# Performance work log

Measured on AMD Instinct MI355X. Metric: run time of the kernel, lower is better.

## Reference

```python
import jax, jax.numpy as jnp
import numpy as np

N, E, F, D = 50000, 800000, 128, 32
CUTOFF = 5.0


def swish(x):
    return x * jax.nn.sigmoid(x)


def setup_inputs() -> dict:
    key = jax.random.key(0)
    ks = jax.random.split(key, 15)
    sF = 1.0 / np.sqrt(F)
    inp = {
        "x": jax.random.normal(ks[0], (N, F), jnp.float32),
        # distances in [0, 6) so some edges lie beyond the 5.0 cutoff
        "rij": jax.random.uniform(ks[1], (E,), jnp.float32) * 6.0,
        "vij": jax.random.normal(ks[2], (E, 3), jnp.float32),
        "src": jax.random.randint(ks[3], (E,), 0, N),
        "dst": jax.random.randint(ks[4], (E,), 0, N),
        # transform: Dense(F,F,swish) -> Dense(F,D,swish)
        "W1": jax.random.normal(ks[5], (F, F), jnp.float32) * sF,
        "b1": jnp.zeros((F,), jnp.float32),
        "W2": jax.random.normal(ks[6], (F, D), jnp.float32) * sF,
        "b2": jnp.zeros((D,), jnp.float32),
        # transform2 (cross_product branch)
        "W1b": jax.random.normal(ks[7], (F, F), jnp.float32) * sF,
        "b1b": jnp.zeros((F,), jnp.float32),
        "W2b": jax.random.normal(ks[8], (F, D), jnp.float32) * sF,
        "b2b": jnp.zeros((D,), jnp.float32),
        # mix: Dense(3, 1), no activation
        "w_mix": jax.random.normal(ks[9], (3,), jnp.float32) * (1.0 / np.sqrt(3.0)),
        "b_mix": jnp.zeros((1,), jnp.float32),
    }
    return inp


def reference(x, rij, vij, src, dst, W1, b1, W2, b2, W1b, b1b, W2b, b2b, w_mix, b_mix):
    # node transforms: q, q2 in [N, D]
    q = swish(swish(x @ W1 + b1) @ W2 + b2)
    q2 = swish(swish(x @ W1b + b1b) @ W2b + b2b)

    # cosine cutoff on per-edge distance [E]
    c = 0.5 * (jnp.cos(jnp.pi * rij / CUTOFF) + 1.0)
    c = c * (rij < CUTOFF).astype(c.dtype)

    # e_mul_u: edge vij [E,1,3] * source-node q [E,D,1] -> [E,D,3], then cutoff scale
    mu_ij = vij[:, None, :] * q[src][:, :, None] * c[:, None, None]
    mu = jax.ops.segment_sum(mu_ij, dst, num_segments=N)  # [N,D,3]

    mu_ij2 = vij[:, None, :] * q2[src][:, :, None] * c[:, None, None]
    mu2 = jax.ops.segment_sum(mu_ij2, dst, num_segments=N)  # [N,D,3]

    mu3 = jnp.cross(mu, mu2, axis=-1)  # [N,D,3]
    stacked = jnp.stack([mu, mu2, mu3], axis=-1)  # [N,D,3,3]
    out = stacked @ w_mix + b_mix[0]  # mix Dense(3,1), squeezed -> [N,D,3]
    return out
```

## Files before the change

kernel.cpp:

```cpp
#include <hip/hip_runtime.h>
#include <hip/hip_bf16.h>

#define N_NODES 50000
#define E_EDGES 800000
#define F_DIM 128
#define D_DIM 32
#define CUTOFF 5.0f
#define PI_F 3.14159265358979f
#define SCAN_BLOCKS ((N_NODES + 255) / 256)

#define MLP_BLOCKS ((N_NODES + 31) / 32)
#define HIST_BLOCKS ((E_EDGES + 255) / 256)
#define XPAD 132
#define SQ_STRIDE 66

__device__ __forceinline__ float swishf(float x) { return x / (1.0f + expf(-x)); }

__global__ __launch_bounds__(256, 4)
void mlp_hist(const float* __restrict__ x,
              const float* __restrict__ W1a, const float* __restrict__ b1a,
              const float* __restrict__ W2a, const float* __restrict__ b2a,
              const float* __restrict__ W1b, const float* __restrict__ b1b,
              const float* __restrict__ W2b, const float* __restrict__ b2b,
              float* __restrict__ qq,
              const float* __restrict__ rij, const int* __restrict__ dst,
              int* __restrict__ deg) {
  if (blockIdx.x >= MLP_BLOCKS) {
    const int e = (blockIdx.x - MLP_BLOCKS) * 256 + threadIdx.x;
    if (e < E_EDGES && rij[e] < CUTOFF) atomicAdd(&deg[dst[e]], 1);
    return;
  }

  __shared__ float sX[64 * XPAD];

  const int rb = blockIdx.x * 32;
  const int t  = threadIdx.x;
  const int w  = t >> 6;
  const int l  = t & 63;

  {
    const int row = t >> 3;
    const int kq  = t & 7;
    const int rowG = min(rb + row, N_NODES - 1);
    const float* xp = x + (size_t)rowG * F_DIM;
#pragma unroll
    for (int p = 0; p < 4; ++p) {
      const int k0 = kq * 4 + p * 32;
      *(float4*)&sX[row * XPAD + k0] = *(const float4*)&xp[k0];
    }
  }
  __syncthreads();

  const int h1    = l >> 5;
  const int cl    = l & 31;
  const int col   = w * 32 + cl;
  const int rbase = h1 * 16;

  float accA[16], accB[16];
  {
    const float bA = b1a[col];
    const float bB = b1b[col];
#pragma unroll
    for (int r = 0; r < 16; ++r) { accA[r] = bA; accB[r] = bB; }
  }
  {
    const float* xrow = sX + rbase * XPAD;
#pragma unroll 2
    for (int k4 = 0; k4 < 32; ++k4) {
      float wa[4], wb[4];
#pragma unroll
      for (int kk = 0; kk < 4; ++kk) {
        const size_t off = (size_t)(k4 * 4 + kk) * F_DIM + col;
        wa[kk] = W1a[off];
        wb[kk] = W1b[off];
      }
#pragma unroll
      for (int r = 0; r < 16; ++r) {
        const float4 xv = *(const float4*)&xrow[r * XPAD + k4 * 4];
        accA[r] = fmaf(xv.x, wa[0], accA[r]);
        accA[r] = fmaf(xv.y, wa[1], accA[r]);
        accA[r] = fmaf(xv.z, wa[2], accA[r]);
        accA[r] = fmaf(xv.w, wa[3], accA[r]);
        accB[r] = fmaf(xv.x, wb[0], accB[r]);
        accB[r] = fmaf(xv.y, wb[1], accB[r]);
        accB[r] = fmaf(xv.z, wb[2], accB[r]);
        accB[r] = fmaf(xv.w, wb[3], accB[r]);
      }
    }
  }

  __syncthreads();
#pragma unroll
  for (int r = 0; r < 16; ++r) {
    sX[(rbase + r) * XPAD + col]      = swishf(accA[r]);
    sX[(32 + rbase + r) * XPAD + col] = swishf(accB[r]);
  }
  __syncthreads();

  const int s   = w * 16 + (l & 15);
  const int rq  = l >> 4;
  const int br2 = s >> 5;
  const int c2  = s & 31;

  const float* __restrict__ W2 = br2 ? W2b : W2a;
  const float* hbase = sX + (br2 ? 32 : 0) * XPAD + (rq * 8) * XPAD;

  float acc2[8];
  {
    const float b2v = (br2 ? b2b : b2a)[c2];
#pragma unroll
    for (int r = 0; r < 8; ++r) acc2[r] = b2v;
  }
#pragma unroll 2
  for (int k4 = 0; k4 < 32; ++k4) {
    float w2v[4];
#pragma unroll
    for (int kk = 0; kk < 4; ++kk)
      w2v[kk] = W2[(size_t)(k4 * 4 + kk) * D_DIM + c2];
#pragma unroll
    for (int r = 0; r < 8; ++r) {
      const float4 hv = *(const float4*)&hbase[r * XPAD + k4 * 4];
      acc2[r] = fmaf(hv.x, w2v[0], acc2[r]);
      acc2[r] = fmaf(hv.y, w2v[1], acc2[r]);
      acc2[r] = fmaf(hv.z, w2v[2], acc2[r]);
      acc2[r] = fmaf(hv.w, w2v[3], acc2[r]);
    }
  }

  __syncthreads();
#pragma unroll
  for (int r = 0; r < 8; ++r)
    sX[(rq * 8 + r) * SQ_STRIDE + 2 * c2 + br2] = swishf(acc2[r]);
  __syncthreads();

  {
    const int row = t >> 3;
    const int m   = t & 7;
    if (rb + row < N_NODES) {
      const float* sq = &sX[row * SQ_STRIDE + m * 8];
      float4 v0 = *(const float4*)&sq[0];
      float4 v1 = *(const float4*)&sq[4];
      float* qp = &qq[(size_t)(rb + row) * 64 + m * 8];
      *(float4*)&qp[0] = v0;
      *(float4*)&qp[4] = v1;
    }
  }
}

__global__ __launch_bounds__(256)
void scan_blocksum(const int* __restrict__ deg, int* __restrict__ part) {
  __shared__ int red[256];
  const int t = threadIdx.x;
  const int i = blockIdx.x * 256 + t;
  red[t] = (i < N_NODES) ? deg[i] : 0;
  __syncthreads();
#pragma unroll
  for (int off = 128; off > 0; off >>= 1) {
    if (t < off) red[t] += red[t + off];
    __syncthreads();
  }
  if (t == 0) part[blockIdx.x] = red[0];
}

__global__ __launch_bounds__(256)
void scan_finish(const int* __restrict__ deg, const int* __restrict__ part,
                 int* __restrict__ row_start, int* __restrict__ cursor) {
  __shared__ int sp[256];
  __shared__ int s[256];
  const int t = threadIdx.x;
  sp[t] = (t < SCAN_BLOCKS) ? part[t] : 0;
  __syncthreads();
  for (int off = 1; off < 256; off <<= 1) {
    const int u = (t >= off) ? sp[t - off] : 0;
    __syncthreads();
    sp[t] += u;
    __syncthreads();
  }
  const int bofs = (blockIdx.x > 0) ? sp[blockIdx.x - 1] : 0;
  if (blockIdx.x == 0 && t == 0) row_start[N_NODES] = sp[SCAN_BLOCKS - 1];

  const int i = blockIdx.x * 256 + t;
  const int v = (i < N_NODES) ? deg[i] : 0;
  s[t] = v;
  __syncthreads();
  for (int off = 1; off < 256; off <<= 1) {
    const int u = (t >= off) ? s[t - off] : 0;
    __syncthreads();
    s[t] += u;
    __syncthreads();
  }
  const int excl = s[t] - v + bofs;
  if (i < N_NODES) { row_start[i] = excl; cursor[i] = excl; }
}

__global__ __launch_bounds__(256)
void edge_reorder(const float* __restrict__ rij, const float* __restrict__ vij,
                  const int* __restrict__ src, const int* __restrict__ dst,
                  int* __restrict__ cursor, float4* __restrict__ recs) {
  const int e = blockIdx.x * 256 + threadIdx.x;
  if (e >= E_EDGES) return;
  const float r = rij[e];
  if (r >= CUTOFF) return;
  const float c = 0.5f * (cosf(r * (PI_F / CUTOFF)) + 1.0f);
  const int pos = atomicAdd(&cursor[dst[e]], 1);
  recs[pos] = make_float4(c * vij[3 * e + 0], c * vij[3 * e + 1],
                          c * vij[3 * e + 2], __int_as_float(src[e]));
}

__global__ __launch_bounds__(256)
void gather_out(const int* __restrict__ row_start, const float4* __restrict__ recs,
                const float2* __restrict__ qq,
                const float* __restrict__ w_mix, const float* __restrict__ b_mix,
                float* __restrict__ out) {
  const int tid = blockIdx.x * 256 + threadIdx.x;
  const int n = tid >> 5;
  const int d = tid & 31;
  if (n >= N_NODES) return;

  const int s0 = row_start[n];
  const int s1 = row_start[n + 1];

  float ax = 0.f, ay = 0.f, az = 0.f, bx = 0.f, by = 0.f, bz = 0.f;
  for (int i = s0; i < s1; i += 4) {
    const int i1 = min(i + 1, s1 - 1);
    const int i2 = min(i + 2, s1 - 1);
    const int i3 = min(i + 3, s1 - 1);
    float4 rc0 = recs[i];
    float4 rc1 = recs[i1];
    float4 rc2 = recs[i2];
    float4 rc3 = recs[i3];
    float2 p0 = qq[__float_as_int(rc0.w) * 32 + d];
    float2 p1 = qq[__float_as_int(rc1.w) * 32 + d];
    float2 p2 = qq[__float_as_int(rc2.w) * 32 + d];
    float2 p3 = qq[__float_as_int(rc3.w) * 32 + d];
    const float m1 = (i + 1 < s1) ? 1.f : 0.f;
    const float m2 = (i + 2 < s1) ? 1.f : 0.f;
    const float m3 = (i + 3 < s1) ? 1.f : 0.f;
    p1.x *= m1; p1.y *= m1;
    p2.x *= m2; p2.y *= m2;
    p3.x *= m3; p3.y *= m3;

    ax += rc0.x * p0.x + rc1.x * p1.x + rc2.x * p2.x + rc3.x * p3.x;
    ay += rc0.y * p0.x + rc1.y * p1.x + rc2.y * p2.x + rc3.y * p3.x;
    az += rc0.z * p0.x + rc1.z * p1.x + rc2.z * p2.x + rc3.z * p3.x;
    bx += rc0.x * p0.y + rc1.x * p1.y + rc2.x * p2.y + rc3.x * p3.y;
    by += rc0.y * p0.y + rc1.y * p1.y + rc2.y * p2.y + rc3.y * p3.y;
    bz += rc0.z * p0.y + rc1.z * p1.y + rc2.z * p2.y + rc3.z * p3.y;
  }

  const float cx = ay * bz - az * by;
  const float cy = az * bx - ax * bz;
  const float cz = ax * by - ay * bx;

  const float w0 = w_mix[0], w1 = w_mix[1], w2 = w_mix[2];
  const float bm = b_mix[0];

  const size_t base = (size_t)tid * 3;
  out[base + 0] = ax * w0 + bx * w1 + cx * w2 + bm;
  out[base + 1] = ay * w0 + by * w1 + cy * w2 + bm;
  out[base + 2] = az * w0 + bz * w1 + cz * w2 + bm;
}

extern "C" void kernel_launch(void* const* d_in, const int* in_sizes, int n_in,
                              void* d_out, int out_size, void* d_ws, size_t ws_size,
                              hipStream_t stream) {
  const float* x     = (const float*)d_in[0];
  const float* rij   = (const float*)d_in[1];
  const float* vij   = (const float*)d_in[2];
  const int*   src   = (const int*)  d_in[3];
  const int*   dst   = (const int*)  d_in[4];
  const float* W1    = (const float*)d_in[5];
  const float* b1    = (const float*)d_in[6];
  const float* W2    = (const float*)d_in[7];
  const float* b2    = (const float*)d_in[8];
  const float* W1b   = (const float*)d_in[9];
  const float* b1b   = (const float*)d_in[10];
  const float* W2b   = (const float*)d_in[11];
  const float* b2b   = (const float*)d_in[12];
  const float* w_mix = (const float*)d_in[13];
  const float* b_mix = (const float*)d_in[14];
  float* out = (float*)d_out;

  float4* recs   = (float4*)d_ws;
  float* qq      = (float*)(recs + E_EDGES);
  int* deg       = (int*)(qq + (size_t)N_NODES * 64);
  int* cursor    = deg + N_NODES;
  int* row_start = cursor + N_NODES;
  int* part      = row_start + N_NODES + 1;

  hipMemsetAsync(deg, 0, sizeof(int) * N_NODES, stream);

  mlp_hist<<<MLP_BLOCKS + HIST_BLOCKS, 256, 0, stream>>>(
      x, W1, b1, W2, b2, W1b, b1b, W2b, b2b, qq, rij, dst, deg);

  scan_blocksum<<<SCAN_BLOCKS, 256, 0, stream>>>(deg, part);
  scan_finish<<<SCAN_BLOCKS, 256, 0, stream>>>(deg, part, row_start, cursor);

  const int eb = (E_EDGES + 255) / 256;
  edge_reorder<<<eb, 256, 0, stream>>>(rij, vij, src, dst, cursor, recs);

  gather_out<<<(N_NODES * D_DIM) / 256, 256, 0, stream>>>(
      row_start, recs, (const float2*)qq, w_mix, b_mix, out);
}
```

Measured before the change: 285.4 us.

## Run node MLP on bf16 MFMA with split hi/lo precision emulation

Replaces the scalar FP32 FMA loops of both MLP layers with MFMA 16x16x32 bf16 matrix instructions. Accuracy is kept close to fp32 by splitting each operand into bf16 hi and lo parts and using three MFMAs per tile. A new prep kernel converts and transposes the weights into hi/lo bf16 buffers and also zeroes the degree array, replacing the memset. The weight buffers live in the workspace region aliased with the tail of the edge-record buffer, which is safe only because edge_reorder writes recs after the MLP has run.

New measurement: 240.2 us. 15.8% less time.

```diff
diff --git a/kernel.cpp b/kernel.cpp
--- a/kernel.cpp
+++ b/kernel.cpp
@@ -11,17 +11,53 @@
 
 #define MLP_BLOCKS ((N_NODES + 31) / 32)
 #define HIST_BLOCKS ((E_EDGES + 255) / 256)
-#define XPAD 132
-#define SQ_STRIDE 66
+#define XS 136
+#define HS 264
+
+typedef __attribute__((ext_vector_type(8))) short bf16x8;
+typedef __attribute__((ext_vector_type(4))) float f32x4;
 
 __device__ __forceinline__ float swishf(float x) { return x / (1.0f + expf(-x)); }
+
+__device__ __forceinline__ unsigned short f2bf(float v) {
+  unsigned u = __float_as_uint(v);
+  u += 0x7FFFu + ((u >> 16) & 1u);
+  return (unsigned short)(u >> 16);
+}
+__device__ __forceinline__ float bf2f(unsigned short h) {
+  return __uint_as_float(((unsigned)h) << 16);
+}
+
+__global__ __launch_bounds__(256)
+void prep(const float* __restrict__ W1a, const float* __restrict__ W1b,
+          const float* __restrict__ W2a, const float* __restrict__ W2b,
+          unsigned short* __restrict__ w1hi, unsigned short* __restrict__ w1lo,
+          unsigned short* __restrict__ w2hi, unsigned short* __restrict__ w2lo,
+          int* __restrict__ deg) {
+  const int id = blockIdx.x * 256 + threadIdx.x;
+  if (id < N_NODES) deg[id] = 0;
+  if (id < 2 * 128 * 128) {
+    const int b = id >> 14, rem = id & 16383, c = rem >> 7, k = rem & 127;
+    const float v = (b ? W1b : W1a)[k * F_DIM + c];
+    const unsigned short h = f2bf(v);
+    w1hi[id] = h;
+    w1lo[id] = f2bf(v - bf2f(h));
+  }
+  if (id < 2 * 32 * 128) {
+    const int b = id >> 12, rem = id & 4095, c = rem >> 7, k = rem & 127;
+    const float v = (b ? W2b : W2a)[k * D_DIM + c];
+    const unsigned short h = f2bf(v);
+    w2hi[id] = h;
+    w2lo[id] = f2bf(v - bf2f(h));
+  }
+}
 
 __global__ __launch_bounds__(256, 4)
 void mlp_hist(const float* __restrict__ x,
-              const float* __restrict__ W1a, const float* __restrict__ b1a,
-              const float* __restrict__ W2a, const float* __restrict__ b2a,
-              const float* __restrict__ W1b, const float* __restrict__ b1b,
-              const float* __restrict__ W2b, const float* __restrict__ b2b,
+              const unsigned short* __restrict__ w1hi, const unsigned short* __restrict__ w1lo,
+              const unsigned short* __restrict__ w2hi, const unsigned short* __restrict__ w2lo,
+              const float* __restrict__ b1a, const float* __restrict__ b1b,
+              const float* __restrict__ b2a, const float* __restrict__ b2b,
               float* __restrict__ qq,
               const float* __restrict__ rij, const int* __restrict__ dst,
               int* __restrict__ deg) {
@@ -31,12 +67,17 @@
     return;
   }
 
-  __shared__ float sX[64 * XPAD];
+  __shared__ unsigned short sU[2 * 32 * HS];
 
   const int rb = blockIdx.x * 32;
   const int t  = threadIdx.x;
   const int w  = t >> 6;
   const int l  = t & 63;
+  const int lr = l & 15;
+  const int kb = l >> 4;
+
+  unsigned short* xh = sU;
+  unsigned short* xl = sU + 32 * XS;
 
   {
     const int row = t >> 3;
@@ -46,100 +87,120 @@
 #pragma unroll
     for (int p = 0; p < 4; ++p) {
       const int k0 = kq * 4 + p * 32;
-      *(float4*)&sX[row * XPAD + k0] = *(const float4*)&xp[k0];
-    }
-  }
-  __syncthreads();
-
-  const int h1    = l >> 5;
-  const int cl    = l & 31;
-  const int col   = w * 32 + cl;
-  const int rbase = h1 * 16;
-
-  float accA[16], accB[16];
+      const float4 v = *(const float4*)&xp[k0];
+      ushort4 hi4, lo4;
+      hi4.x = f2bf(v.x); lo4.x = f2bf(v.x - bf2f(hi4.x));
+      hi4.y = f2bf(v.y); lo4.y = f2bf(v.y - bf2f(hi4.y));
+      hi4.z = f2bf(v.z); lo4.z = f2bf(v.z - bf2f(hi4.z));
+      hi4.w = f2bf(v.w); lo4.w = f2bf(v.w - bf2f(hi4.w));
+      *(ushort4*)&xh[row * XS + k0] = hi4;
+      *(ushort4*)&xl[row * XS + k0] = lo4;
+    }
+  }
+  __syncthreads();
+
+  f32x4 acc[2][4];
+#pragma unroll
+  for (int mt = 0; mt < 2; ++mt)
+#pragma unroll
+    for (int ct = 0; ct < 4; ++ct) acc[mt][ct] = (f32x4){0.f, 0.f, 0.f, 0.f};
+
+#pragma unroll
+  for (int ks = 0; ks < 4; ++ks) {
+    bf16x8 ah[2], al[2];
+#pragma unroll
+    for (int mt = 0; mt < 2; ++mt) {
+      ah[mt] = *(const bf16x8*)&xh[(mt * 16 + lr) * XS + ks * 32 + kb * 8];
+      al[mt] = *(const bf16x8*)&xl[(mt * 16 + lr) * XS + ks * 32 + kb * 8];
+    }
+#pragma unroll
+    for (int ct = 0; ct < 4; ++ct) {
+      const int cb = w * 64 + ct * 16;
+      const size_t wo = (size_t)(cb + lr) * 128 + ks * 32 + kb * 8;
+      const bf16x8 bh = *(const bf16x8*)&w1hi[wo];
+      const bf16x8 bl = *(const bf16x8*)&w1lo[wo];
+#pragma unroll
+      for (int mt = 0; mt < 2; ++mt) {
+        acc[mt][ct] = __builtin_amdgcn_mfma_f32_16x16x32_bf16(ah[mt], bh, acc[mt][ct], 0, 0, 0);
+        acc[mt][ct] = __builtin_amdgcn_mfma_f32_16x16x32_bf16(ah[mt], bl, acc[mt][ct], 0, 0, 0);
+        acc[mt][ct] = __builtin_amdgcn_mfma_f32_16x16x32_bf16(al[mt], bh, acc[mt][ct], 0, 0, 0);
+      }
+    }
+  }
+
+  __syncthreads();
+  unsigned short* hh = sU;
+  unsigned short* hl = sU + 32 * HS;
+
   {
-    const float bA = b1a[col];
-    const float bB = b1b[col];
-#pragma unroll
-    for (int r = 0; r < 16; ++r) { accA[r] = bA; accB[r] = bB; }
-  }
-  {
-    const float* xrow = sX + rbase * XPAD;
-#pragma unroll 2
-    for (int k4 = 0; k4 < 32; ++k4) {
-      float wa[4], wb[4];
-#pragma unroll
-      for (int kk = 0; kk < 4; ++kk) {
-        const size_t off = (size_t)(k4 * 4 + kk) * F_DIM + col;
-        wa[kk] = W1a[off];
-        wb[kk] = W1b[off];
+    const float* b1p = (w >= 2) ? b1b : b1a;
+#pragma unroll
+    for (int ct = 0; ct < 4; ++ct) {
+      const int colc = w * 64 + ct * 16 + lr;
+      const float bias = b1p[colc & 127];
+#pragma unroll
+      for (int mt = 0; mt < 2; ++mt) {
+#pragma unroll
+        for (int rg = 0; rg < 4; ++rg) {
+          const int rowr = mt * 16 + kb * 4 + rg;
+          const float hv = swishf(acc[mt][ct][rg] + bias);
+          const unsigned short hb = f2bf(hv);
+          hh[rowr * HS + colc] = hb;
+          hl[rowr * HS + colc] = f2bf(hv - bf2f(hb));
+        }
       }
-#pragma unroll
-      for (int r = 0; r < 16; ++r) {
-        const float4 xv = *(const float4*)&xrow[r * XPAD + k4 * 4];
-        accA[r] = fmaf(xv.x, wa[0], accA[r]);
-        accA[r] = fmaf(xv.y, wa[1], accA[r]);
-        accA[r] = fmaf(xv.z, wa[2], accA[r]);
-        accA[r] = fmaf(xv.w, wa[3], accA[r]);
-        accB[r] = fmaf(xv.x, wb[0], accB[r]);
-        accB[r] = fmaf(xv.y, wb[1], accB[r]);
-        accB[r] = fmaf(xv.z, wb[2], accB[r]);
-        accB[r] = fmaf(xv.w, wb[3], accB[r]);
-      }
-    }
-  }
-
-  __syncthreads();
-#pragma unroll
-  for (int r = 0; r < 16; ++r) {
-    sX[(rbase + r) * XPAD + col]      = swishf(accA[r]);
-    sX[(32 + rbase + r) * XPAD + col] = swishf(accB[r]);
-  }
-  __syncthreads();
-
-  const int s   = w * 16 + (l & 15);
-  const int rq  = l >> 4;
-  const int br2 = s >> 5;
-  const int c2  = s & 31;
-
-  const float* __restrict__ W2 = br2 ? W2b : W2a;
-  const float* hbase = sX + (br2 ? 32 : 0) * XPAD + (rq * 8) * XPAD;
-
-  float acc2[8];
+    }
+  }
+  __syncthreads();
+
+  const int cb2 = 16 * w;
+  const int br2 = cb2 >> 5;
+  const int c2  = (cb2 & 31) + lr;
+
+  f32x4 acc2[2];
+  acc2[0] = (f32x4){0.f, 0.f, 0.f, 0.f};
+  acc2[1] = (f32x4){0.f, 0.f, 0.f, 0.f};
+#pragma unroll
+  for (int ks = 0; ks < 4; ++ks) {
+    bf16x8 ah2[2], al2[2];
+#pragma unroll
+    for (int mt = 0; mt < 2; ++mt) {
+      const int ho = (mt * 16 + lr) * HS + br2 * 128 + ks * 32 + kb * 8;
+      ah2[mt] = *(const bf16x8*)&hh[ho];
+      al2[mt] = *(const bf16x8*)&hl[ho];
+    }
+    const size_t w2o = (size_t)(br2 * 32 + c2) * 128 + ks * 32 + kb * 8;
+    const bf16x8 bh2 = *(const bf16x8*)&w2hi[w2o];
+    const bf16x8 bl2 = *(const bf16x8*)&w2lo[w2o];
+#pragma unroll
+    for (int mt = 0; mt < 2; ++mt) {
+      acc2[mt] = __builtin_amdgcn_mfma_f32_16x16x32_bf16(ah2[mt], bh2, acc2[mt], 0, 0, 0);
+      acc2[mt] = __builtin_amdgcn_mfma_f32_16x16x32_bf16(ah2[mt], bl2, acc2[mt], 0, 0, 0);
+      acc2[mt] = __builtin_amdgcn_mfma_f32_16x16x32_bf16(al2[mt], bh2, acc2[mt], 0, 0, 0);
+    }
+  }
+
+  __syncthreads();
+  float* sQ = (float*)sU;
   {
     const float b2v = (br2 ? b2b : b2a)[c2];
 #pragma unroll
-    for (int r = 0; r < 8; ++r) acc2[r] = b2v;
-  }
-#pragma unroll 2
-  for (int k4 = 0; k4 < 32; ++k4) {
-    float w2v[4];
-#pragma unroll
-    for (int kk = 0; kk < 4; ++kk)
-      w2v[kk] = W2[(size_t)(k4 * 4 + kk) * D_DIM + c2];
-#pragma unroll
-    for (int r = 0; r < 8; ++r) {
-      const float4 hv = *(const float4*)&hbase[r * XPAD + k4 * 4];
-      acc2[r] = fmaf(hv.x, w2v[0], acc2[r]);
-      acc2[r] = fmaf(hv.y, w2v[1], acc2[r]);
-      acc2[r] = fmaf(hv.z, w2v[2], acc2[r]);
-      acc2[r] = fmaf(hv.w, w2v[3], acc2[r]);
-    }
-  }
-
-  __syncthreads();
-#pragma unroll
-  for (int r = 0; r < 8; ++r)
-    sX[(rq * 8 + r) * SQ_STRIDE + 2 * c2 + br2] = swishf(acc2[r]);
+    for (int mt = 0; mt < 2; ++mt)
+#pragma unroll
+      for (int rg = 0; rg < 4; ++rg) {
+        const int rowr = mt * 16 + kb * 4 + rg;
+        sQ[rowr * 66 + 2 * c2 + br2] = swishf(acc2[mt][rg] + b2v);
+      }
+  }
   __syncthreads();
 
   {
     const int row = t >> 3;
     const int m   = t & 7;
     if (rb + row < N_NODES) {
-      const float* sq = &sX[row * SQ_STRIDE + m * 8];
-      float4 v0 = *(const float4*)&sq[0];
-      float4 v1 = *(const float4*)&sq[4];
+      const float* sq = &sQ[row * 66 + m * 8];
+      const float4 v0 = *(const float4*)&sq[0];
+      const float4 v1 = *(const float4*)&sq[4];
       float* qp = &qq[(size_t)(rb + row) * 64 + m * 8];
       *(float4*)&qp[0] = v0;
       *(float4*)&qp[4] = v1;
@@ -288,10 +349,16 @@
   int* row_start = cursor + N_NODES;
   int* part      = row_start + N_NODES + 1;
 
-  hipMemsetAsync(deg, 0, sizeof(int) * N_NODES, stream);
+  unsigned short* w1hi = (unsigned short*)(recs + 760000);
+  unsigned short* w1lo = w1hi + 2 * 128 * 128;
+  unsigned short* w2hi = w1lo + 2 * 128 * 128;
+  unsigned short* w2lo = w2hi + 2 * 32 * 128;
+
+  prep<<<SCAN_BLOCKS, 256, 0, stream>>>(W1, W1b, W2, W2b,
+                                        w1hi, w1lo, w2hi, w2lo, deg);
 
   mlp_hist<<<MLP_BLOCKS + HIST_BLOCKS, 256, 0, stream>>>(
-      x, W1, b1, W2, b2, W1b, b1b, W2b, b2b, qq, rij, dst, deg);
+      x, w1hi, w1lo, w2hi, w2lo, b1, b1b, b2, b2b, qq, rij, dst, deg);
 
   scan_blocksum<<<SCAN_BLOCKS, 256, 0, stream>>>(deg, part);
   scan_finish<<<SCAN_BLOCKS, 256, 0, stream>>>(deg, part, row_start, cursor);
```
